# Kernel tuning notes

Measured on AMD Instinct MI355X. Metric: run time of the kernel, lower is better.

The kernel has to match this reference:

```python
import jax, jax.numpy as jnp
import numpy as np

D_MODEL = 1024
H = 16
D_K = D_MODEL // H
B, S = 2, 2048
NEG = -1e9


def setup_inputs() -> dict:
    key = jax.random.key(0)
    ks = jax.random.split(key, 8)
    scale = 1.0 / np.sqrt(D_MODEL)
    q = jax.random.normal(ks[0], (B, S, D_MODEL), dtype=jnp.float32)
    k = jax.random.normal(ks[1], (B, S, D_MODEL), dtype=jnp.float32)
    v = jax.random.normal(ks[2], (B, S, D_MODEL), dtype=jnp.float32)
    # causal 0/1 mask, broadcastable to [B, h, S, S]
    mask = jnp.tril(jnp.ones((S, S), dtype=jnp.int32))[None, None, :, :]
    w_q = jax.random.normal(ks[3], (D_MODEL, D_MODEL), dtype=jnp.float32) * scale
    w_k = jax.random.normal(ks[4], (D_MODEL, D_MODEL), dtype=jnp.float32) * scale
    w_v = jax.random.normal(ks[5], (D_MODEL, D_MODEL), dtype=jnp.float32) * scale
    w_o = jax.random.normal(ks[6], (D_MODEL, D_MODEL), dtype=jnp.float32) * scale
    return {"q": q, "k": k, "v": v, "mask": mask,
            "w_q": w_q, "w_k": w_k, "w_v": w_v, "w_o": w_o}


def reference(q, k, v, mask, w_q, w_k, w_v, w_o):
    # projections (no bias)
    def split_heads(x):
        Bn, Sn, _ = x.shape
        return x.reshape(Bn, Sn, H, D_K).transpose(0, 2, 1, 3)  # [B,h,S,d_k]

    qh = split_heads(q @ w_q)
    kh = split_heads(k @ w_k)
    vh = split_heads(v @ w_v)

    scores = jnp.einsum('bhqd,bhkd->bhqk', qh, kh) / jnp.sqrt(
        jnp.asarray(D_K, dtype=qh.dtype))
    scores = jnp.where(mask == 0, jnp.asarray(NEG, dtype=scores.dtype), scores)
    attn = jax.nn.softmax(scores, axis=-1)  # dropout rate 0.0 -> identity
    x = jnp.einsum('bhqk,bhkd->bhqd', attn, vh)  # [B,h,S,d_k]
    x = x.transpose(0, 2, 1, 3).reshape(q.shape[0], q.shape[1], D_MODEL)
    return x @ w_o
```

## Files before the change

### kernel.cpp

```cpp
#include <hip/hip_runtime.h>

#define D_MODEL 1024
#define NH 16
#define DK 64
#define BB 2
#define SS 2048
#define M_TOT (BB*SS)

typedef float f32x4 __attribute__((ext_vector_type(4)));
typedef float f32x16 __attribute__((ext_vector_type(16)));
typedef __bf16 bf16x8 __attribute__((ext_vector_type(8)));
typedef unsigned int u32;

#define QSCALE 0.1803368801f
#define DEFER_THR 11.5416f

__device__ __forceinline__ unsigned short f2bf(float f){
  unsigned int u = __float_as_uint(f);
  unsigned int r = (u + 0x7fffu + ((u >> 16) & 1u)) >> 16;
  return (unsigned short)r;
}

__device__ __forceinline__ void gload_lds16(const void* g, void* l){
  __builtin_amdgcn_global_load_lds((const __attribute__((address_space(1))) void*)g,
                                   (__attribute__((address_space(3))) void*)l,
                                   16, 0, 0);
}

__device__ __forceinline__ void swap_half(u32 a, u32 b, int hi, u32& x, u32& y){
#if __has_builtin(__builtin_amdgcn_permlane32_swap)
  typedef unsigned int uint2v __attribute__((ext_vector_type(2)));
  uint2v r = __builtin_amdgcn_permlane32_swap(a, b, false, false);
  x = r.x; y = r.y;
#else
  u32 as = __shfl_xor(a, 32);
  u32 bs = __shfl_xor(b, 32);
  x = hi ? bs : a;
  y = hi ? b  : as;
#endif
}

__global__ __launch_bounds__(256) void cvt3_bf16(const float* __restrict__ q,
                                                 const float* __restrict__ k,
                                                 const float* __restrict__ v,
                                                 unsigned short* __restrict__ qb,
                                                 unsigned short* __restrict__ kb,
                                                 unsigned short* __restrict__ vb){
  const int which = blockIdx.y;
  const float* in = (which == 0) ? q : (which == 1) ? k : v;
  unsigned short* out = (which == 0) ? qb : (which == 1) ? kb : vb;
  int i = blockIdx.x * 256 + threadIdx.x;
  float4 f = ((const float4*)in)[i];
  ushort4 o;
  o.x = f2bf(f.x); o.y = f2bf(f.y); o.z = f2bf(f.z); o.w = f2bf(f.w);
  ((ushort4*)out)[i] = o;
}

__global__ __launch_bounds__(256) void transpose_cvt4(const float* __restrict__ wq,
                                                      const float* __restrict__ wk,
                                                      const float* __restrict__ wv,
                                                      const float* __restrict__ wo,
                                                      unsigned short* __restrict__ WqkvT,
                                                      unsigned short* __restrict__ woT){
  __shared__ float tile[64][65];
  const int which = blockIdx.z;
  const float* w = (which == 0) ? wq : (which == 1) ? wk : (which == 2) ? wv : wo;
  unsigned short* wt = (which == 3) ? woT : (WqkvT + (size_t)which * 1024 * 1024);
  const int N = D_MODEL;
  const int bx = blockIdx.x * 64;
  const int by = blockIdx.y * 64;
  const int t = threadIdx.x;
  #pragma unroll
  for (int i = 0; i < 16; ++i){
    int idx = t + i * 256;
    int r = idx >> 6, c = idx & 63;
    tile[r][c] = w[(size_t)(by + r) * N + bx + c];
  }
  __syncthreads();
  #pragma unroll
  for (int i = 0; i < 16; ++i){
    int idx = t + i * 256;
    int r = idx >> 6, c = idx & 63;
    wt[(size_t)(bx + r) * N + by + c] = f2bf(tile[c][r]);
  }
}

__global__ __launch_bounds__(256) void gemm_qkv(const unsigned short* __restrict__ Aq,
                                                const unsigned short* __restrict__ Ak,
                                                const unsigned short* __restrict__ Av,
                                                const unsigned short* __restrict__ WT,
                                                unsigned short* __restrict__ Qh,
                                                unsigned short* __restrict__ Kh,
                                                unsigned short* __restrict__ VhT){
  __shared__ unsigned short Al[2][128 * 32];
  __shared__ unsigned short Bl[2][128 * 32];
  const int tid = threadIdx.x;
  const int wid = tid >> 6, lane = tid & 63;
  const int lr = lane & 15, lg = lane >> 4;
  const int wm = wid >> 1, wn = wid & 1;
  const int bm = blockIdx.x, bn = blockIdx.y;
  const int seg = bn >> 3;
  const unsigned short* A = (seg == 0) ? Aq : (seg == 1) ? Ak : Av;
  const int K = D_MODEL;

  f32x4 acc[4][4];
  #pragma unroll
  for (int i = 0; i < 4; ++i)
    #pragma unroll
    for (int j = 0; j < 4; ++j)
      acc[i][j] = (f32x4){0.f, 0.f, 0.f, 0.f};

  auto stage = [&](int buf, int kt){
    #pragma unroll
    for (int r = 0; r < 2; ++r){
      int vt = tid + r * 256;
      int row = vt >> 2, c8 = (vt & 3) * 8;
      gload_lds16(A  + (size_t)(bm * 128 + row) * K + kt * 32 + c8,
                  &Al[buf][(wid << 9) + r * 2048]);
      gload_lds16(WT + (size_t)(bn * 128 + row) * K + kt * 32 + c8,
                  &Bl[buf][(wid << 9) + r * 2048]);
    }
  };

  stage(0, 0);
  int cur = 0;
  for (int kt = 0; kt < 32; ++kt){
    __syncthreads();
    if (kt + 1 < 32) stage(cur ^ 1, kt + 1);
    bf16x8 af[4], bfr[4];
    #pragma unroll
    for (int i = 0; i < 4; ++i)
      af[i] = *(const bf16x8*)&Al[cur][(wm * 64 + i * 16 + lr) * 32 + lg * 8];
    #pragma unroll
    for (int j = 0; j < 4; ++j)
      bfr[j] = *(const bf16x8*)&Bl[cur][(wn * 64 + j * 16 + lr) * 32 + lg * 8];
    #pragma unroll
    for (int i = 0; i < 4; ++i)
      #pragma unroll
      for (int j = 0; j < 4; ++j)
        acc[i][j] = __builtin_amdgcn_mfma_f32_16x16x32_bf16(af[i], bfr[j], acc[i][j], 0, 0, 0);
    cur ^= 1;
  }

  if (seg < 2){
    unsigned short* O = (seg == 0) ? Qh : Kh;
    const float sc = (seg == 0) ? QSCALE : 1.0f;
    #pragma unroll
    for (int i = 0; i < 4; ++i){
      int row0 = bm * 128 + wm * 64 + i * 16 + lg * 4;
      #pragma unroll
      for (int j = 0; j < 4; ++j){
        int colseg = (bn & 7) * 128 + wn * 64 + j * 16 + lr;
        int h = colseg >> 6, dk = colseg & 63;
        #pragma unroll
        for (int p = 0; p < 4; ++p){
          int rowm = row0 + p;
          int b = rowm >> 11, s = rowm & 2047;
          O[((size_t)(b * NH + h) * SS + s) * DK + dk] = f2bf(acc[i][j][p] * sc);
        }
      }
    }
  } else {
    #pragma unroll
    for (int i = 0; i < 4; ++i){
      int row0 = bm * 128 + wm * 64 + i * 16 + lg * 4;
      int b = row0 >> 11, s = row0 & 2047;
      #pragma unroll
      for (int j = 0; j < 4; ++j){
        int colseg = (bn & 7) * 128 + wn * 64 + j * 16 + lr;
        int h = colseg >> 6, dk = colseg & 63;
        ushort4 o4;
        o4.x = f2bf(acc[i][j][0]); o4.y = f2bf(acc[i][j][1]);
        o4.z = f2bf(acc[i][j][2]); o4.w = f2bf(acc[i][j][3]);
        *(ushort4*)&VhT[((size_t)(b * NH + h) * DK + dk) * SS + s] = o4;
      }
    }
  }
}

__global__ __launch_bounds__(256) void gemm_o64(const unsigned short* __restrict__ A,
                                                const unsigned short* __restrict__ Bt,
                                                float* __restrict__ O){
  __shared__ unsigned short Al[2][64 * 32];
  __shared__ unsigned short Bl[2][128 * 32];
  const int tid = threadIdx.x;
  const int wid = tid >> 6, lane = tid & 63;
  const int lr = lane & 15, lg = lane >> 4;
  const int wm = wid >> 1, wn = wid & 1;
  const int bm = blockIdx.x, bn = blockIdx.y;
  const int K = D_MODEL;

  f32x4 acc[2][4];
  #pragma unroll
  for (int i = 0; i < 2; ++i)
    #pragma unroll
    for (int j = 0; j < 4; ++j)
      acc[i][j] = (f32x4){0.f, 0.f, 0.f, 0.f};

  auto stage = [&](int buf, int kt){
    {
      int row = tid >> 2, c8 = (tid & 3) * 8;
      gload_lds16(A + (size_t)(bm * 64 + row) * K + kt * 32 + c8,
                  &Al[buf][wid << 9]);
    }
    #pragma unroll
    for (int r = 0; r < 2; ++r){
      int vt = tid + r * 256;
      int row = vt >> 2, c8 = (vt & 3) * 8;
      gload_lds16(Bt + (size_t)(bn * 128 + row) * K + kt * 32 + c8,
                  &Bl[buf][(wid << 9) + r * 2048]);
    }
  };

  stage(0, 0);
  int cur = 0;
  for (int kt = 0; kt < 32; ++kt){
    __syncthreads();
    if (kt + 1 < 32) stage(cur ^ 1, kt + 1);
    bf16x8 af[2], bfr[4];
    #pragma unroll
    for (int i = 0; i < 2; ++i)
      af[i] = *(const bf16x8*)&Al[cur][(wm * 32 + i * 16 + lr) * 32 + lg * 8];
    #pragma unroll
    for (int j = 0; j < 4; ++j)
      bfr[j] = *(const bf16x8*)&Bl[cur][(wn * 64 + j * 16 + lr) * 32 + lg * 8];
    #pragma unroll
    for (int i = 0; i < 2; ++i)
      #pragma unroll
      for (int j = 0; j < 4; ++j)
        acc[i][j] = __builtin_amdgcn_mfma_f32_16x16x32_bf16(af[i], bfr[j], acc[i][j], 0, 0, 0);
    cur ^= 1;
  }

  #pragma unroll
  for (int i = 0; i < 2; ++i){
    int row0 = bm * 64 + wm * 32 + i * 16 + lg * 4;
    #pragma unroll
    for (int j = 0; j < 4; ++j){
      int col = bn * 128 + wn * 64 + j * 16 + lr;
      #pragma unroll
      for (int p = 0; p < 4; ++p)
        O[(size_t)(row0 + p) * D_MODEL + col] = acc[i][j][p];
    }
  }
}

__global__ __launch_bounds__(128) void attn_kernel(const unsigned short* __restrict__ Qh,
                                                   const unsigned short* __restrict__ Kh,
                                                   const unsigned short* __restrict__ VhT,
                                                   unsigned short* __restrict__ Oc){
  __shared__ unsigned short Kl[2][64 * 64];
  __shared__ unsigned short Vl[2][64 * 64];
  const int bh = blockIdx.x;
  const int qblk = 31 - blockIdx.y;
  const int tid = threadIdx.x, wid = tid >> 6, lane = tid & 63;
  const int ln = lane & 31, hi = lane >> 5;
  const int b = bh >> 4, h = bh & 15;
  const size_t kvbase = (size_t)bh * SS * DK;
  const int q0 = qblk * 64 + wid * 32;
  const int Tw = qblk * 2 + wid;
  const int NT = qblk + 1;

  const unsigned short* qp = Qh + kvbase + (size_t)(q0 + ln) * DK + hi * 8;
  bf16x8 qbv[4];
  #pragma unroll
  for (int c = 0; c < 4; ++c) qbv[c] = *(const bf16x8*)(qp + c * 16);

  f32x16 oa0 = {0,0,0,0,0,0,0,0,0,0,0,0,0,0,0,0};
  f32x16 oa1 = {0,0,0,0,0,0,0,0,0,0,0,0,0,0,0,0};
  float m = -1e30f, ls = 0.f;

  auto stage = [&](int buf, int t){
    const int k0 = t * 64;
    #pragma unroll
    for (int r = 0; r < 4; ++r){
      const int row = r * 16 + (tid >> 3);
      const int slot = (tid & 7) ^ (row & 7);
      gload_lds16(Kh  + kvbase + (size_t)(k0 + row) * DK + slot * 8,
                  &Kl[buf][r * 1024 + wid * 512]);
      gload_lds16(VhT + kvbase + (size_t)row * SS + k0 + slot * 8,
                  &Vl[buf][r * 1024 + wid * 512]);
    }
  };

  stage(0, 0);
  int cur = 0;
  #pragma unroll 1
  for (int t = 0; t < NT; ++t){
    __syncthreads();
    if (t + 1 < NT) stage(cur ^ 1, t + 1);
    const unsigned short* Kb = Kl[cur];
    const unsigned short* Vb = Vl[cur];

    f32x16 sta = {0,0,0,0,0,0,0,0,0,0,0,0,0,0,0,0};
    f32x16 stb = {0,0,0,0,0,0,0,0,0,0,0,0,0,0,0,0};
    __builtin_amdgcn_s_setprio(1);
    #pragma unroll
    for (int c = 0; c < 4; ++c){
      const int po = ((c * 2 + hi) ^ (ln & 7)) * 8;
      bf16x8 kfa = *(const bf16x8*)&Kb[ln * 64 + po];
      bf16x8 kfb = *(const bf16x8*)&Kb[(32 + ln) * 64 + po];
      sta = __builtin_amdgcn_mfma_f32_32x32x16_bf16(kfa, qbv[c], sta, 0, 0, 0);
      stb = __builtin_amdgcn_mfma_f32_32x32x16_bf16(kfb, qbv[c], stb, 0, 0, 0);
    }
    __builtin_amdgcn_s_setprio(0);

    const int ta = 2 * t, tb = 2 * t + 1;
    if (tb == Tw){
      #pragma unroll
      for (int r = 0; r < 16; ++r){
        int kg = (r & 3) + 8 * (r >> 2) + 4 * hi;
        if (kg > ln) stb[r] = -1e30f;
      }
    } else if (ta == Tw){
      #pragma unroll
      for (int r = 0; r < 16; ++r){
        int kg = (r & 3) + 8 * (r >> 2) + 4 * hi;
        if (kg > ln) sta[r] = -1e30f;
        stb[r] = -1e30f;
      }
    }

    float tm[8];
    #pragma unroll
    for (int i = 0; i < 8; ++i)
      tm[i] = fmaxf(fmaxf(sta[2*i], sta[2*i+1]), fmaxf(stb[2*i], stb[2*i+1]));
    float mx = fmaxf(fmaxf(fmaxf(tm[0], tm[1]), fmaxf(tm[2], tm[3])),
                     fmaxf(fmaxf(tm[4], tm[5]), fmaxf(tm[6], tm[7])));
    mx = fmaxf(mx, __shfl_xor(mx, 32));

    if (__any(mx > m + DEFER_THR)){
      const float mn = fmaxf(m, mx);
      const float fac = __builtin_amdgcn_exp2f(m - mn);
      m = mn;
      ls *= fac;
      #pragma unroll
      for (int r = 0; r < 16; ++r){ oa0[r] *= fac; oa1[r] *= fac; }
    }

    #pragma unroll
    for (int r = 0; r < 16; ++r){
      sta[r] = __builtin_amdgcn_exp2f(sta[r] - m);
      stb[r] = __builtin_amdgcn_exp2f(stb[r] - m);
    }
    float sm[8];
    #pragma unroll
    for (int i = 0; i < 8; ++i)
      sm[i] = (sta[2*i] + sta[2*i+1]) + (stb[2*i] + stb[2*i+1]);
    float rs = ((sm[0] + sm[1]) + (sm[2] + sm[3])) + ((sm[4] + sm[5]) + (sm[6] + sm[7]));
    rs += __shfl_xor(rs, 32);
    ls += rs;

    u32 ca[8], cb[8];
    #pragma unroll
    for (int i = 0; i < 8; ++i){
      asm("v_cvt_pk_bf16_f32 %0, %1, %2" : "=v"(ca[i]) : "v"(sta[2*i]), "v"(sta[2*i+1]));
      asm("v_cvt_pk_bf16_f32 %0, %1, %2" : "=v"(cb[i]) : "v"(stb[2*i]), "v"(stb[2*i+1]));
    }
    u32 w0[4], w1[4], w2[4], w3[4];
    swap_half(ca[0], ca[2], hi, w0[0], w0[2]);
    swap_half(ca[1], ca[3], hi, w0[1], w0[3]);
    swap_half(ca[4], ca[6], hi, w1[0], w1[2]);
    swap_half(ca[5], ca[7], hi, w1[1], w1[3]);
    swap_half(cb[0], cb[2], hi, w2[0], w2[2]);
    swap_half(cb[1], cb[3], hi, w2[1], w2[3]);
    swap_half(cb[4], cb[6], hi, w3[0], w3[2]);
    swap_half(cb[5], cb[7], hi, w3[1], w3[3]);
    bf16x8 pf[4];
    __builtin_memcpy(&pf[0], w0, 16);
    __builtin_memcpy(&pf[1], w1, 16);
    __builtin_memcpy(&pf[2], w2, 16);
    __builtin_memcpy(&pf[3], w3, 16);

    __builtin_amdgcn_s_setprio(1);
    #pragma unroll
    for (int ks = 0; ks < 4; ++ks){
      const int po = ((ks * 2 + hi) ^ (ln & 7)) * 8;
      bf16x8 v0 = *(const bf16x8*)&Vb[ln * 64 + po];
      bf16x8 v1 = *(const bf16x8*)&Vb[(32 + ln) * 64 + po];
      oa0 = __builtin_amdgcn_mfma_f32_32x32x16_bf16(v0, pf[ks], oa0, 0, 0, 0);
      oa1 = __builtin_amdgcn_mfma_f32_32x32x16_bf16(v1, pf[ks], oa1, 0, 0, 0);
    }
    __builtin_amdgcn_s_setprio(0);
    cur ^= 1;
  }

  const float inv = 1.0f / ls;
  const size_t rowbase = ((size_t)b * SS + q0 + ln) * D_MODEL + h * DK;
  #pragma unroll
  for (int g = 0; g < 4; ++g){
    ushort4 o4;
    o4.x = f2bf(oa0[4*g + 0] * inv); o4.y = f2bf(oa0[4*g + 1] * inv);
    o4.z = f2bf(oa0[4*g + 2] * inv); o4.w = f2bf(oa0[4*g + 3] * inv);
    *(ushort4*)&Oc[rowbase + 8*g + 4*hi] = o4;
  }
  #pragma unroll
  for (int g = 0; g < 4; ++g){
    ushort4 o4;
    o4.x = f2bf(oa1[4*g + 0] * inv); o4.y = f2bf(oa1[4*g + 1] * inv);
    o4.z = f2bf(oa1[4*g + 2] * inv); o4.w = f2bf(oa1[4*g + 3] * inv);
    *(ushort4*)&Oc[rowbase + 32 + 8*g + 4*hi] = o4;
  }
}

extern "C" void kernel_launch(void* const* d_in, const int* in_sizes, int n_in,
                              void* d_out, int out_size, void* d_ws, size_t ws_size,
                              hipStream_t stream){
  const float* q  = (const float*)d_in[0];
  const float* k  = (const float*)d_in[1];
  const float* v  = (const float*)d_in[2];
  const float* wq = (const float*)d_in[4];
  const float* wk = (const float*)d_in[5];
  const float* wv = (const float*)d_in[6];
  const float* wo = (const float*)d_in[7];
  float* out = (float*)d_out;

  char* ws = (char*)d_ws;
  const size_t MB = 1024 * 1024;
  unsigned short* qb     = (unsigned short*)(ws + 0 * MB);
  unsigned short* kb     = (unsigned short*)(ws + 8 * MB);
  unsigned short* vb     = (unsigned short*)(ws + 16 * MB);
  unsigned short* WqkvT  = (unsigned short*)(ws + 24 * MB);
  unsigned short* woT    = (unsigned short*)(ws + 30 * MB);
  unsigned short* Qh     = (unsigned short*)(ws + 32 * MB);
  unsigned short* Kh     = (unsigned short*)(ws + 40 * MB);
  unsigned short* VhT    = (unsigned short*)(ws + 48 * MB);
  unsigned short* attnb  = (unsigned short*)(ws + 56 * MB);

  const int n4 = (M_TOT * D_MODEL) / 4;
  dim3 gc(n4 / 256, 3);
  cvt3_bf16<<<gc, 256, 0, stream>>>(q, k, v, qb, kb, vb);

  dim3 tg(16, 16, 4);
  transpose_cvt4<<<tg, 256, 0, stream>>>(wq, wk, wv, wo, WqkvT, woT);

  dim3 gqkv(M_TOT / 128, 3 * D_MODEL / 128);
  gemm_qkv<<<gqkv, 256, 0, stream>>>(qb, kb, vb, WqkvT, Qh, Kh, VhT);

  dim3 ga(BB * NH, SS / 64);
  attn_kernel<<<ga, 128, 0, stream>>>(Qh, Kh, VhT, attnb);

  dim3 go(M_TOT / 64, D_MODEL / 128);
  gemm_o64<<<go, 256, 0, stream>>>(attnb, woT, out);
}
```

Baseline: 137.3 us.

## Split KV range across two wave pairs in attention with LDS merge

Doubles the attention block to four waves, where two wave pairs process alternating KV tiles for the same 64 query rows. Each pair keeps its own online-softmax state, and the partial results are merged through shared memory at the end. This aims to raise parallelism and occupancy per query block. In exchange it drops the double-buffered prefetch, adds a barrier per round, and adds a final LDS reduction.

```diff
diff --git a/kernel.cpp b/kernel.cpp
--- a/kernel.cpp
+++ b/kernel.cpp
@@ -245,21 +245,21 @@
   }
 }
 
-__global__ __launch_bounds__(128) void attn_kernel(const unsigned short* __restrict__ Qh,
+__global__ __launch_bounds__(256) void attn_kernel(const unsigned short* __restrict__ Qh,
                                                    const unsigned short* __restrict__ Kh,
                                                    const unsigned short* __restrict__ VhT,
                                                    unsigned short* __restrict__ Oc){
-  __shared__ unsigned short Kl[2][64 * 64];
-  __shared__ unsigned short Vl[2][64 * 64];
+  __shared__ unsigned short SL[4][4096];
   const int bh = blockIdx.x;
   const int qblk = 31 - blockIdx.y;
   const int tid = threadIdx.x, wid = tid >> 6, lane = tid & 63;
   const int ln = lane & 31, hi = lane >> 5;
+  const int qh = wid & 1, pp = wid >> 1;
   const int b = bh >> 4, h = bh & 15;
   const size_t kvbase = (size_t)bh * SS * DK;
-  const int q0 = qblk * 64 + wid * 32;
-  const int Tw = qblk * 2 + wid;
-  const int NT = qblk + 1;
+  const int q0 = qblk * 64 + qh * 32;
+  const int Tw = 2 * qblk + qh;
+  const int R = (qblk + 2) >> 1;
 
   const unsigned short* qp = Qh + kvbase + (size_t)(q0 + ln) * DK + hi * 8;
   bf16x8 qbv[4];
@@ -270,136 +270,165 @@
   f32x16 oa1 = {0,0,0,0,0,0,0,0,0,0,0,0,0,0,0,0};
   float m = -1e30f, ls = 0.f;
 
-  auto stage = [&](int buf, int t){
-    const int k0 = t * 64;
-    #pragma unroll
-    for (int r = 0; r < 4; ++r){
-      const int row = r * 16 + (tid >> 3);
-      const int slot = (tid & 7) ^ (row & 7);
-      gload_lds16(Kh  + kvbase + (size_t)(k0 + row) * DK + slot * 8,
-                  &Kl[buf][r * 1024 + wid * 512]);
-      gload_lds16(VhT + kvbase + (size_t)row * SS + k0 + slot * 8,
-                  &Vl[buf][r * 1024 + wid * 512]);
-    }
-  };
-
-  stage(0, 0);
-  int cur = 0;
   #pragma unroll 1
-  for (int t = 0; t < NT; ++t){
+  for (int r = 0; r < R; ++r){
+    {
+      const int k0A = (2 * r) * 64;
+      const int k0B = k0A + 64;
+      const bool haveB = (2 * r + 1) <= qblk;
+      #pragma unroll
+      for (int i = 0; i < 2; ++i){
+        const int c = i * 256 + tid;
+        const int row = c >> 3;
+        const int slot = (c & 7) ^ (row & 7);
+        const int ldso = (i * 256 + wid * 64) * 8;
+        gload_lds16(Kh  + kvbase + (size_t)(k0A + row) * DK + slot * 8, &SL[0][ldso]);
+        gload_lds16(VhT + kvbase + (size_t)row * SS + k0A + slot * 8,   &SL[1][ldso]);
+        if (haveB){
+          gload_lds16(Kh  + kvbase + (size_t)(k0B + row) * DK + slot * 8, &SL[2][ldso]);
+          gload_lds16(VhT + kvbase + (size_t)row * SS + k0B + slot * 8,   &SL[3][ldso]);
+        }
+      }
+    }
     __syncthreads();
-    if (t + 1 < NT) stage(cur ^ 1, t + 1);
-    const unsigned short* Kb = Kl[cur];
-    const unsigned short* Vb = Vl[cur];
-
-    f32x16 sta = {0,0,0,0,0,0,0,0,0,0,0,0,0,0,0,0};
-    f32x16 stb = {0,0,0,0,0,0,0,0,0,0,0,0,0,0,0,0};
-    __builtin_amdgcn_s_setprio(1);
-    #pragma unroll
-    for (int c = 0; c < 4; ++c){
-      const int po = ((c * 2 + hi) ^ (ln & 7)) * 8;
-      bf16x8 kfa = *(const bf16x8*)&Kb[ln * 64 + po];
-      bf16x8 kfb = *(const bf16x8*)&Kb[(32 + ln) * 64 + po];
-      sta = __builtin_amdgcn_mfma_f32_32x32x16_bf16(kfa, qbv[c], sta, 0, 0, 0);
-      stb = __builtin_amdgcn_mfma_f32_32x32x16_bf16(kfb, qbv[c], stb, 0, 0, 0);
-    }
-    __builtin_amdgcn_s_setprio(0);
-
-    const int ta = 2 * t, tb = 2 * t + 1;
-    if (tb == Tw){
-      #pragma unroll
-      for (int r = 0; r < 16; ++r){
-        int kg = (r & 3) + 8 * (r >> 2) + 4 * hi;
-        if (kg > ln) stb[r] = -1e30f;
-      }
-    } else if (ta == Tw){
-      #pragma unroll
-      for (int r = 0; r < 16; ++r){
-        int kg = (r & 3) + 8 * (r >> 2) + 4 * hi;
-        if (kg > ln) sta[r] = -1e30f;
-        stb[r] = -1e30f;
-      }
-    }
-
-    float tm[8];
-    #pragma unroll
-    for (int i = 0; i < 8; ++i)
-      tm[i] = fmaxf(fmaxf(sta[2*i], sta[2*i+1]), fmaxf(stb[2*i], stb[2*i+1]));
-    float mx = fmaxf(fmaxf(fmaxf(tm[0], tm[1]), fmaxf(tm[2], tm[3])),
-                     fmaxf(fmaxf(tm[4], tm[5]), fmaxf(tm[6], tm[7])));
-    mx = fmaxf(mx, __shfl_xor(mx, 32));
-
-    if (__any(mx > m + DEFER_THR)){
-      const float mn = fmaxf(m, mx);
-      const float fac = __builtin_amdgcn_exp2f(m - mn);
-      m = mn;
-      ls *= fac;
-      #pragma unroll
-      for (int r = 0; r < 16; ++r){ oa0[r] *= fac; oa1[r] *= fac; }
-    }
-
-    #pragma unroll
-    for (int r = 0; r < 16; ++r){
-      sta[r] = __builtin_amdgcn_exp2f(sta[r] - m);
-      stb[r] = __builtin_amdgcn_exp2f(stb[r] - m);
-    }
-    float sm[8];
-    #pragma unroll
-    for (int i = 0; i < 8; ++i)
-      sm[i] = (sta[2*i] + sta[2*i+1]) + (stb[2*i] + stb[2*i+1]);
-    float rs = ((sm[0] + sm[1]) + (sm[2] + sm[3])) + ((sm[4] + sm[5]) + (sm[6] + sm[7]));
-    rs += __shfl_xor(rs, 32);
-    ls += rs;
-
-    u32 ca[8], cb[8];
-    #pragma unroll
-    for (int i = 0; i < 8; ++i){
-      asm("v_cvt_pk_bf16_f32 %0, %1, %2" : "=v"(ca[i]) : "v"(sta[2*i]), "v"(sta[2*i+1]));
-      asm("v_cvt_pk_bf16_f32 %0, %1, %2" : "=v"(cb[i]) : "v"(stb[2*i]), "v"(stb[2*i+1]));
-    }
-    u32 w0[4], w1[4], w2[4], w3[4];
-    swap_half(ca[0], ca[2], hi, w0[0], w0[2]);
-    swap_half(ca[1], ca[3], hi, w0[1], w0[3]);
-    swap_half(ca[4], ca[6], hi, w1[0], w1[2]);
-    swap_half(ca[5], ca[7], hi, w1[1], w1[3]);
-    swap_half(cb[0], cb[2], hi, w2[0], w2[2]);
-    swap_half(cb[1], cb[3], hi, w2[1], w2[3]);
-    swap_half(cb[4], cb[6], hi, w3[0], w3[2]);
-    swap_half(cb[5], cb[7], hi, w3[1], w3[3]);
-    bf16x8 pf[4];
-    __builtin_memcpy(&pf[0], w0, 16);
-    __builtin_memcpy(&pf[1], w1, 16);
-    __builtin_memcpy(&pf[2], w2, 16);
-    __builtin_memcpy(&pf[3], w3, 16);
-
-    __builtin_amdgcn_s_setprio(1);
-    #pragma unroll
-    for (int ks = 0; ks < 4; ++ks){
-      const int po = ((ks * 2 + hi) ^ (ln & 7)) * 8;
-      bf16x8 v0 = *(const bf16x8*)&Vb[ln * 64 + po];
-      bf16x8 v1 = *(const bf16x8*)&Vb[(32 + ln) * 64 + po];
-      oa0 = __builtin_amdgcn_mfma_f32_32x32x16_bf16(v0, pf[ks], oa0, 0, 0, 0);
-      oa1 = __builtin_amdgcn_mfma_f32_32x32x16_bf16(v1, pf[ks], oa1, 0, 0, 0);
-    }
-    __builtin_amdgcn_s_setprio(0);
-    cur ^= 1;
-  }
-
-  const float inv = 1.0f / ls;
-  const size_t rowbase = ((size_t)b * SS + q0 + ln) * D_MODEL + h * DK;
-  #pragma unroll
-  for (int g = 0; g < 4; ++g){
-    ushort4 o4;
-    o4.x = f2bf(oa0[4*g + 0] * inv); o4.y = f2bf(oa0[4*g + 1] * inv);
-    o4.z = f2bf(oa0[4*g + 2] * inv); o4.w = f2bf(oa0[4*g + 3] * inv);
-    *(ushort4*)&Oc[rowbase + 8*g + 4*hi] = o4;
-  }
-  #pragma unroll
-  for (int g = 0; g < 4; ++g){
-    ushort4 o4;
-    o4.x = f2bf(oa1[4*g + 0] * inv); o4.y = f2bf(oa1[4*g + 1] * inv);
-    o4.z = f2bf(oa1[4*g + 2] * inv); o4.w = f2bf(oa1[4*g + 3] * inv);
-    *(ushort4*)&Oc[rowbase + 32 + 8*g + 4*hi] = o4;
+
+    const int t = 2 * r + pp;
+    if (t <= qblk){
+      const unsigned short* Kb = SL[pp * 2];
+      const unsigned short* Vb = SL[pp * 2 + 1];
+
+      f32x16 sta = {0,0,0,0,0,0,0,0,0,0,0,0,0,0,0,0};
+      f32x16 stb = {0,0,0,0,0,0,0,0,0,0,0,0,0,0,0,0};
+      __builtin_amdgcn_s_setprio(1);
+      #pragma unroll
+      for (int c = 0; c < 4; ++c){
+        const int po = ((c * 2 + hi) ^ (ln & 7)) * 8;
+        bf16x8 kfa = *(const bf16x8*)&Kb[ln * 64 + po];
+        bf16x8 kfb = *(const bf16x8*)&Kb[(32 + ln) * 64 + po];
+        sta = __builtin_amdgcn_mfma_f32_32x32x16_bf16(kfa, qbv[c], sta, 0, 0, 0);
+        stb = __builtin_amdgcn_mfma_f32_32x32x16_bf16(kfb, qbv[c], stb, 0, 0, 0);
+      }
+      __builtin_amdgcn_s_setprio(0);
+
+      const int ta = 2 * t, tb = 2 * t + 1;
+      if (tb == Tw){
+        #pragma unroll
+        for (int rr = 0; rr < 16; ++rr){
+          int kg = (rr & 3) + 8 * (rr >> 2) + 4 * hi;
+          if (kg > ln) stb[rr] = -1e30f;
+        }
+      } else if (ta == Tw){
+        #pragma unroll
+        for (int rr = 0; rr < 16; ++rr){
+          int kg = (rr & 3) + 8 * (rr >> 2) + 4 * hi;
+          if (kg > ln) sta[rr] = -1e30f;
+          stb[rr] = -1e30f;
+        }
+      }
+
+      float tm[8];
+      #pragma unroll
+      for (int i = 0; i < 8; ++i)
+        tm[i] = fmaxf(fmaxf(sta[2*i], sta[2*i+1]), fmaxf(stb[2*i], stb[2*i+1]));
+      float mx = fmaxf(fmaxf(fmaxf(tm[0], tm[1]), fmaxf(tm[2], tm[3])),
+                       fmaxf(fmaxf(tm[4], tm[5]), fmaxf(tm[6], tm[7])));
+      mx = fmaxf(mx, __shfl_xor(mx, 32));
+
+      if (__any(mx > m + DEFER_THR)){
+        const float mn = fmaxf(m, mx);
+        const float fac = __builtin_amdgcn_exp2f(m - mn);
+        m = mn;
+        ls *= fac;
+        #pragma unroll
+        for (int rr = 0; rr < 16; ++rr){ oa0[rr] *= fac; oa1[rr] *= fac; }
+      }
+
+      #pragma unroll
+      for (int rr = 0; rr < 16; ++rr){
+        sta[rr] = __builtin_amdgcn_exp2f(sta[rr] - m);
+        stb[rr] = __builtin_amdgcn_exp2f(stb[rr] - m);
+      }
+      float sm[8];
+      #pragma unroll
+      for (int i = 0; i < 8; ++i)
+        sm[i] = (sta[2*i] + sta[2*i+1]) + (stb[2*i] + stb[2*i+1]);
+      float rsum = ((sm[0] + sm[1]) + (sm[2] + sm[3])) + ((sm[4] + sm[5]) + (sm[6] + sm[7]));
+      rsum += __shfl_xor(rsum, 32);
+      ls += rsum;
+
+      u32 ca[8], cb[8];
+      #pragma unroll
+      for (int i = 0; i < 8; ++i){
+        asm("v_cvt_pk_bf16_f32 %0, %1, %2" : "=v"(ca[i]) : "v"(sta[2*i]), "v"(sta[2*i+1]));
+        asm("v_cvt_pk_bf16_f32 %0, %1, %2" : "=v"(cb[i]) : "v"(stb[2*i]), "v"(stb[2*i+1]));
+      }
+      u32 w0[4], w1[4], w2[4], w3[4];
+      swap_half(ca[0], ca[2], hi, w0[0], w0[2]);
+      swap_half(ca[1], ca[3], hi, w0[1], w0[3]);
+      swap_half(ca[4], ca[6], hi, w1[0], w1[2]);
+      swap_half(ca[5], ca[7], hi, w1[1], w1[3]);
+      swap_half(cb[0], cb[2], hi, w2[0], w2[2]);
+      swap_half(cb[1], cb[3], hi, w2[1], w2[3]);
+      swap_half(cb[4], cb[6], hi, w3[0], w3[2]);
+      swap_half(cb[5], cb[7], hi, w3[1], w3[3]);
+      bf16x8 pf[4];
+      __builtin_memcpy(&pf[0], w0, 16);
+      __builtin_memcpy(&pf[1], w1, 16);
+      __builtin_memcpy(&pf[2], w2, 16);
+      __builtin_memcpy(&pf[3], w3, 16);
+
+      __builtin_amdgcn_s_setprio(1);
+      #pragma unroll
+      for (int ks = 0; ks < 4; ++ks){
+        const int po = ((ks * 2 + hi) ^ (ln & 7)) * 8;
+        bf16x8 v0 = *(const bf16x8*)&Vb[ln * 64 + po];
+        bf16x8 v1 = *(const bf16x8*)&Vb[(32 + ln) * 64 + po];
+        oa0 = __builtin_amdgcn_mfma_f32_32x32x16_bf16(v0, pf[ks], oa0, 0, 0, 0);
+        oa1 = __builtin_amdgcn_mfma_f32_32x32x16_bf16(v1, pf[ks], oa1, 0, 0, 0);
+      }
+      __builtin_amdgcn_s_setprio(0);
+    }
+    __syncthreads();
+  }
+
+  float* oL  = (float*)&SL[0][0];
+  float* mLs = (float*)&SL[2][0];
+  if (wid >= 2){
+    const int w = wid - 2;
+    #pragma unroll
+    for (int rr = 0; rr < 16; ++rr){
+      oL[(w * 32 + rr) * 64 + lane]      = oa0[rr];
+      oL[(w * 32 + 16 + rr) * 64 + lane] = oa1[rr];
+    }
+    if (hi == 0){ mLs[w * 32 + ln] = m; mLs[64 + w * 32 + ln] = ls; }
+  }
+  __syncthreads();
+  if (wid < 2){
+    const float m1  = mLs[wid * 32 + ln];
+    const float ls1 = mLs[64 + wid * 32 + ln];
+    const float mstar = fmaxf(m, m1);
+    const float f0 = __builtin_amdgcn_exp2f(m  - mstar);
+    const float f1 = __builtin_amdgcn_exp2f(m1 - mstar);
+    const float inv = 1.0f / (f0 * ls + f1 * ls1);
+    const size_t rowbase = ((size_t)b * SS + q0 + ln) * D_MODEL + h * DK;
+    #pragma unroll
+    for (int g = 0; g < 4; ++g){
+      ushort4 o4;
+      o4.x = f2bf((f0 * oa0[4*g + 0] + f1 * oL[(wid * 32 + 4*g + 0) * 64 + lane]) * inv);
+      o4.y = f2bf((f0 * oa0[4*g + 1] + f1 * oL[(wid * 32 + 4*g + 1) * 64 + lane]) * inv);
+      o4.z = f2bf((f0 * oa0[4*g + 2] + f1 * oL[(wid * 32 + 4*g + 2) * 64 + lane]) * inv);
+      o4.w = f2bf((f0 * oa0[4*g + 3] + f1 * oL[(wid * 32 + 4*g + 3) * 64 + lane]) * inv);
+      *(ushort4*)&Oc[rowbase + 8*g + 4*hi] = o4;
+    }
+    #pragma unroll
+    for (int g = 0; g < 4; ++g){
+      ushort4 o4;
+      o4.x = f2bf((f0 * oa1[4*g + 0] + f1 * oL[(wid * 32 + 16 + 4*g + 0) * 64 + lane]) * inv);
+      o4.y = f2bf((f0 * oa1[4*g + 1] + f1 * oL[(wid * 32 + 16 + 4*g + 1) * 64 + lane]) * inv);
+      o4.z = f2bf((f0 * oa1[4*g + 2] + f1 * oL[(wid * 32 + 16 + 4*g + 2) * 64 + lane]) * inv);
+      o4.w = f2bf((f0 * oa1[4*g + 3] + f1 * oL[(wid * 32 + 16 + 4*g + 3) * 64 + lane]) * inv);
+      *(ushort4*)&Oc[rowbase + 32 + 8*g + 4*hi] = o4;
+    }
   }
 }
 
@@ -438,7 +467,7 @@
   gemm_qkv<<<gqkv, 256, 0, stream>>>(qb, kb, vb, WqkvT, Qh, Kh, VhT);
 
   dim3 ga(BB * NH, SS / 64);
-  attn_kernel<<<ga, 128, 0, stream>>>(Qh, Kh, VhT, attnb);
+  attn_kernel<<<ga, 256, 0, stream>>>(Qh, Kh, VhT, attnb);
 
   dim3 go(M_TOT / 64, D_MODEL / 128);
   gemm_o64<<<go, 256, 0, stream>>>(attnb, woT, out);
```

Measured after the change: 121.5 us. 1.13x faster.

## Split attention into single-wave blocks of 32 query rows without double buffering

Applied to the files above, without the earlier changes.

The attention kernel now launches one 64-thread wave per block covering 32 query rows, which doubles the grid and removes the block-level __syncthreads. Each wave loads its own K/V tile into a single LDS buffer and waits for it synchronously before computing. Previously a double-buffered prefetch was shared by two waves. This raises occupancy and removes inter-wave barriers, but it loses load/compute overlap within a block and doubles global K/V traffic, since each wave fetches its tiles separately.

```diff
diff --git a/kernel.cpp b/kernel.cpp
--- a/kernel.cpp
+++ b/kernel.cpp
@@ -245,21 +245,20 @@
   }
 }
 
-__global__ __launch_bounds__(128) void attn_kernel(const unsigned short* __restrict__ Qh,
-                                                   const unsigned short* __restrict__ Kh,
-                                                   const unsigned short* __restrict__ VhT,
-                                                   unsigned short* __restrict__ Oc){
-  __shared__ unsigned short Kl[2][64 * 64];
-  __shared__ unsigned short Vl[2][64 * 64];
+__global__ __launch_bounds__(64) void attn_kernel(const unsigned short* __restrict__ Qh,
+                                                  const unsigned short* __restrict__ Kh,
+                                                  const unsigned short* __restrict__ VhT,
+                                                  unsigned short* __restrict__ Oc){
+  __shared__ unsigned short SL[2][4096];
   const int bh = blockIdx.x;
-  const int qblk = 31 - blockIdx.y;
-  const int tid = threadIdx.x, wid = tid >> 6, lane = tid & 63;
+  const int qt = 63 - blockIdx.y;
+  const int lane = threadIdx.x & 63;
   const int ln = lane & 31, hi = lane >> 5;
   const int b = bh >> 4, h = bh & 15;
   const size_t kvbase = (size_t)bh * SS * DK;
-  const int q0 = qblk * 64 + wid * 32;
-  const int Tw = qblk * 2 + wid;
-  const int NT = qblk + 1;
+  const int q0 = qt * 32;
+  const int Tw = qt;
+  const int NS = (qt + 2) >> 1;
 
   const unsigned short* qp = Qh + kvbase + (size_t)(q0 + ln) * DK + hi * 8;
   bf16x8 qbv[4];
@@ -270,27 +269,21 @@
   f32x16 oa1 = {0,0,0,0,0,0,0,0,0,0,0,0,0,0,0,0};
   float m = -1e30f, ls = 0.f;
 
-  auto stage = [&](int buf, int t){
-    const int k0 = t * 64;
-    #pragma unroll
-    for (int r = 0; r < 4; ++r){
-      const int row = r * 16 + (tid >> 3);
-      const int slot = (tid & 7) ^ (row & 7);
-      gload_lds16(Kh  + kvbase + (size_t)(k0 + row) * DK + slot * 8,
-                  &Kl[buf][r * 1024 + wid * 512]);
-      gload_lds16(VhT + kvbase + (size_t)row * SS + k0 + slot * 8,
-                  &Vl[buf][r * 1024 + wid * 512]);
-    }
-  };
-
-  stage(0, 0);
-  int cur = 0;
   #pragma unroll 1
-  for (int t = 0; t < NT; ++t){
-    __syncthreads();
-    if (t + 1 < NT) stage(cur ^ 1, t + 1);
-    const unsigned short* Kb = Kl[cur];
-    const unsigned short* Vb = Vl[cur];
+  for (int s = 0; s < NS; ++s){
+    const int k0 = s * 64;
+    asm volatile("s_waitcnt lgkmcnt(0)" ::: "memory");
+    #pragma unroll
+    for (int i = 0; i < 8; ++i){
+      const int row = i * 8 + (lane >> 3);
+      const int slot = (lane & 7) ^ (row & 7);
+      gload_lds16(Kh  + kvbase + (size_t)(k0 + row) * DK + slot * 8, &SL[0][i * 512]);
+      gload_lds16(VhT + kvbase + (size_t)row * SS + k0 + slot * 8,   &SL[1][i * 512]);
+    }
+    asm volatile("s_waitcnt vmcnt(0)" ::: "memory");
+    __builtin_amdgcn_sched_barrier(0);
+    const unsigned short* Kb = SL[0];
+    const unsigned short* Vb = SL[1];
 
     f32x16 sta = {0,0,0,0,0,0,0,0,0,0,0,0,0,0,0,0};
     f32x16 stb = {0,0,0,0,0,0,0,0,0,0,0,0,0,0,0,0};
@@ -305,19 +298,19 @@
     }
     __builtin_amdgcn_s_setprio(0);
 
-    const int ta = 2 * t, tb = 2 * t + 1;
+    const int ta = 2 * s, tb = 2 * s + 1;
     if (tb == Tw){
       #pragma unroll
-      for (int r = 0; r < 16; ++r){
-        int kg = (r & 3) + 8 * (r >> 2) + 4 * hi;
-        if (kg > ln) stb[r] = -1e30f;
+      for (int rr = 0; rr < 16; ++rr){
+        int kg = (rr & 3) + 8 * (rr >> 2) + 4 * hi;
+        if (kg > ln) stb[rr] = -1e30f;
       }
     } else if (ta == Tw){
       #pragma unroll
-      for (int r = 0; r < 16; ++r){
-        int kg = (r & 3) + 8 * (r >> 2) + 4 * hi;
-        if (kg > ln) sta[r] = -1e30f;
-        stb[r] = -1e30f;
+      for (int rr = 0; rr < 16; ++rr){
+        int kg = (rr & 3) + 8 * (rr >> 2) + 4 * hi;
+        if (kg > ln) sta[rr] = -1e30f;
+        stb[rr] = -1e30f;
       }
     }
 
@@ -335,21 +328,21 @@
       m = mn;
       ls *= fac;
       #pragma unroll
-      for (int r = 0; r < 16; ++r){ oa0[r] *= fac; oa1[r] *= fac; }
-    }
-
-    #pragma unroll
-    for (int r = 0; r < 16; ++r){
-      sta[r] = __builtin_amdgcn_exp2f(sta[r] - m);
-      stb[r] = __builtin_amdgcn_exp2f(stb[r] - m);
+      for (int rr = 0; rr < 16; ++rr){ oa0[rr] *= fac; oa1[rr] *= fac; }
+    }
+
+    #pragma unroll
+    for (int rr = 0; rr < 16; ++rr){
+      sta[rr] = __builtin_amdgcn_exp2f(sta[rr] - m);
+      stb[rr] = __builtin_amdgcn_exp2f(stb[rr] - m);
     }
     float sm[8];
     #pragma unroll
     for (int i = 0; i < 8; ++i)
       sm[i] = (sta[2*i] + sta[2*i+1]) + (stb[2*i] + stb[2*i+1]);
-    float rs = ((sm[0] + sm[1]) + (sm[2] + sm[3])) + ((sm[4] + sm[5]) + (sm[6] + sm[7]));
-    rs += __shfl_xor(rs, 32);
-    ls += rs;
+    float rsum = ((sm[0] + sm[1]) + (sm[2] + sm[3])) + ((sm[4] + sm[5]) + (sm[6] + sm[7]));
+    rsum += __shfl_xor(rsum, 32);
+    ls += rsum;
 
     u32 ca[8], cb[8];
     #pragma unroll
@@ -382,7 +375,6 @@
       oa1 = __builtin_amdgcn_mfma_f32_32x32x16_bf16(v1, pf[ks], oa1, 0, 0, 0);
     }
     __builtin_amdgcn_s_setprio(0);
-    cur ^= 1;
   }
 
   const float inv = 1.0f / ls;
@@ -437,8 +429,8 @@
   dim3 gqkv(M_TOT / 128, 3 * D_MODEL / 128);
   gemm_qkv<<<gqkv, 256, 0, stream>>>(qb, kb, vb, WqkvT, Qh, Kh, VhT);
 
-  dim3 ga(BB * NH, SS / 64);
-  attn_kernel<<<ga, 128, 0, stream>>>(Qh, Kh, VhT, attnb);
+  dim3 ga(BB * NH, SS / 32);
+  attn_kernel<<<ga, 64, 0, stream>>>(Qh, Kh, VhT, attnb);
 
   dim3 go(M_TOT / 64, D_MODEL / 128);
   gemm_o64<<<go, 256, 0, stream>>>(attnb, woT, out);
```

Result: no change. 137.3 us (+0.0%).
